# Performance work log

Measured on AMD Instinct MI355X. Metric: run time of the kernel, lower is better.

The kernel has to match this reference:

```python
import jax, jax.numpy as jnp
import numpy as np

N, D = 16384, 2048

def setup_inputs() -> dict:
    key = jax.random.key(0)
    k1, k2 = jax.random.split(key)
    F = jax.random.normal(k1, (N, D), dtype=jnp.float32)
    F_star = jax.random.normal(k2, (N, D), dtype=jnp.float32)
    lambda_r = jnp.float32(1.0)
    return {"F": F, "F_star": F_star, "lambda_r": lambda_r}

def reference(F, F_star, lambda_r):
    # trace(F F^T Fs Fs^T) == ||F^T Fs||_F^2 (cyclic trace property);
    # avoids materializing the n x n Gram matrices the torch code forms.
    G = jnp.einsum('nd,ne->de', F, F_star)  # [D, D]
    return lambda_r * jnp.sum(G * G)
```

## Files before the change

### kernel.cpp

```cpp
#include <hip/hip_runtime.h>
#include <hip/hip_bf16.h>

#define N_ROWS 16384
#define D_DIM  2048
#define SPLITK 4
#define NS     (N_ROWS / 32)
#define NP     (D_DIM / 128)
#define NSS    (NS / SPLITK)
#define NKT    (NSS / 2)


typedef __attribute__((ext_vector_type(8))) short short8;
typedef __attribute__((ext_vector_type(4))) float f32x4;
typedef __attribute__((ext_vector_type(8))) unsigned short ushort8;
typedef __attribute__((ext_vector_type(4))) unsigned short ushort4v;

#define GPTR(p) ((const __attribute__((address_space(1))) void*)(p))
#define LPTR(p) ((__attribute__((address_space(3))) void*)(p))

__device__ __forceinline__ unsigned short f2bf(float x) {
  __hip_bfloat16 b = __float2bfloat16(x);
  return *reinterpret_cast<unsigned short*>(&b);
}
__device__ __forceinline__ float bf2f(unsigned short u) {
  unsigned int v = ((unsigned int)u) << 16;
  return *reinterpret_cast<float*>(&v);
}

__global__ void __launch_bounds__(256) transpose_pack(
    const float* __restrict__ F, const float* __restrict__ Fs,
    unsigned short* __restrict__ Fb, unsigned short* __restrict__ Fsb) {
  const float* src = blockIdx.y ? Fs : F;
  unsigned short* dst = blockIdx.y ? Fsb : Fb;
  const int t = threadIdx.x;
  const int kb0 = blockIdx.x * 64;

  const int mg   = t & 31;
  const int koct = (t >> 5) & 3;
  const int c    = t >> 7;
  const int krow = kb0 + c * 32 + koct * 8;
  const int ks   = blockIdx.x * 2 + c;

  const float* srow = &src[(size_t)krow * D_DIM + mg * 4];
  unsigned short* obase = dst + (size_t)ks * 4096
                        + (size_t)(mg >> 2) * 512 + (size_t)koct * 128
                        + (size_t)(mg & 3) * 32;

#define LOADP(R, MT) do {                                                      \
    _Pragma("unroll") for (int j = 0; j < 8; ++j)                              \
      (R)[j] = *(const float4*)&srow[(size_t)j * D_DIM + (MT) * 128];          \
  } while (0)
#define STOREP(R, MT) do {                                                     \
    const float* _rp = (const float*)(R);                                      \
    unsigned short* _b = obase + (size_t)(MT) * (NS * 4096);                   \
    _Pragma("unroll") for (int i = 0; i < 4; ++i) {                            \
      ushort8 _o;                                                              \
      _Pragma("unroll") for (int j = 0; j < 8; ++j) _o[j] = f2bf(_rp[j*4+i]);  \
      *(ushort8*)&_b[i * 8] = _o;                                              \
    }                                                                          \
  } while (0)

  float4 rA[8], rB[8];
  LOADP(rA, 0);
#pragma unroll
  for (int mt = 0; mt < NP; mt += 2) {
    LOADP(rB, mt + 1);
    STOREP(rA, mt);
    if (mt + 2 < NP) LOADP(rA, mt + 2);
    STOREP(rB, mt + 1);
  }
#undef LOADP
#undef STOREP
}

__global__ void __launch_bounds__(512, 2) gemm_packed(
    const unsigned short* __restrict__ Fb, const unsigned short* __restrict__ Fsb,
    unsigned short* __restrict__ Cpart) {
  __shared__ unsigned short lds[65536];
  const int tid = threadIdx.x;
  const int w = tid >> 6, lane = tid & 63;
  const int wm = w >> 2, wn = w & 3;
  const int bx = blockIdx.x, by = blockIdx.y, z = blockIdx.z;

  const size_t kbase = (size_t)z * NSS * 4096;
  size_t aSrc0 = ((size_t)(by * 2 + 0) * NS) * 4096 + kbase + (size_t)w * 1024 + lane * 8;
  size_t aSrc1 = ((size_t)(by * 2 + 1) * NS) * 4096 + kbase + (size_t)w * 1024 + lane * 8;
  size_t bSrc0 = ((size_t)(bx * 2 + 0) * NS) * 4096 + kbase + (size_t)w * 1024 + lane * 8;
  size_t bSrc1 = ((size_t)(bx * 2 + 1) * NS) * 4096 + kbase + (size_t)w * 1024 + lane * 8;

  const int aRd = wm * 8192 + lane * 8;
  const int bRd = (wn >> 1) * 8192 + (wn & 1) * 2048 + lane * 8;

#define STAGE_A(KT, P, BUF) do {                                               \
    int _kt = (KT); if (_kt >= NKT) _kt -= NKT;                                \
    const unsigned short* _s = Fb + (P ? aSrc1 : aSrc0) + (size_t)_kt * 8192;  \
    unsigned short* _d = &lds[(BUF) * 16384 + (P) * 8192 + w * 1024];          \
    __builtin_amdgcn_global_load_lds(GPTR(_s),       LPTR(_d),       16, 0, 0);\
    __builtin_amdgcn_global_load_lds(GPTR(_s + 512), LPTR(_d + 512), 16, 0, 0);\
  } while (0)
#define STAGE_B(KT, Q, BUF) do {                                               \
    int _kt = (KT); if (_kt >= NKT) _kt -= NKT;                                \
    const unsigned short* _s = Fsb + (Q ? bSrc1 : bSrc0) + (size_t)_kt * 8192; \
    unsigned short* _d = &lds[32768 + (BUF) * 16384 + (Q) * 8192 + w * 1024];  \
    __builtin_amdgcn_global_load_lds(GPTR(_s),       LPTR(_d),       16, 0, 0);\
    __builtin_amdgcn_global_load_lds(GPTR(_s + 512), LPTR(_d + 512), 16, 0, 0);\
  } while (0)
#define LDA(DST, BUF, I, SL) (DST) = *(const short8*)&lds[(BUF) * 16384 + aRd + (SL) * 4096 + (I) * 512]
#define LDB(DST, BUF, J, SL) (DST) = *(const short8*)&lds[32768 + (BUF) * 16384 + bRd + (SL) * 4096 + (J) * 512]

  f32x4 acc[8][4];
#pragma unroll
  for (int i = 0; i < 8; ++i)
#pragma unroll
    for (int j = 0; j < 4; ++j) acc[i][j] = 0.f;

  short8 aR[4][2], bLo[2][2], bHi[2][2];

  STAGE_A(0, 0, 0); STAGE_A(0, 1, 0);
  STAGE_B(0, 0, 0); STAGE_B(0, 1, 0);
  STAGE_B(1, 0, 1); STAGE_B(1, 1, 1);
  asm volatile("s_waitcnt vmcnt(4)" ::: "memory");
  __builtin_amdgcn_s_barrier();

#define PHASE1(T, B) do {                                                      \
    _Pragma("unroll") for (int i = 0; i < 4; ++i) {                            \
      LDA(aR[i][0], B, i, 0); LDA(aR[i][1], B, i, 1); }                        \
    _Pragma("unroll") for (int j = 0; j < 2; ++j) {                            \
      LDB(bLo[j][0], B, j, 0); LDB(bLo[j][1], B, j, 1); }                      \
    STAGE_A((T) + 1, 0, (B) ^ 1);                                              \
    asm volatile("s_waitcnt lgkmcnt(8)" ::: "memory");                         \
    __builtin_amdgcn_s_barrier();                                              \
    asm volatile("s_waitcnt lgkmcnt(0)" ::: "memory");                         \
    __builtin_amdgcn_s_setprio(1);                                             \
    _Pragma("unroll") for (int sl = 0; sl < 2; ++sl)                           \
      _Pragma("unroll") for (int i = 0; i < 4; ++i)                            \
        _Pragma("unroll") for (int j = 0; j < 2; ++j)                          \
          acc[i][j] = __builtin_amdgcn_mfma_f32_16x16x32_bf16(aR[i][sl], bLo[j][sl], acc[i][j], 0, 0, 0); \
    __builtin_amdgcn_s_setprio(0);                                             \
    __builtin_amdgcn_s_barrier();                                              \
  } while (0)
#define PHASE2(T, B) do {                                                      \
    _Pragma("unroll") for (int j = 0; j < 2; ++j) {                            \
      LDB(bHi[j][0], B, 2 + j, 0); LDB(bHi[j][1], B, 2 + j, 1); }              \
    STAGE_A((T) + 1, 1, (B) ^ 1);                                              \
    __builtin_amdgcn_s_barrier();                                              \
    asm volatile("s_waitcnt lgkmcnt(0)" ::: "memory");                         \
    __builtin_amdgcn_s_setprio(1);                                             \
    _Pragma("unroll") for (int sl = 0; sl < 2; ++sl)                           \
      _Pragma("unroll") for (int i = 0; i < 4; ++i)                            \
        _Pragma("unroll") for (int j = 0; j < 2; ++j)                          \
          acc[i][2 + j] = __builtin_amdgcn_mfma_f32_16x16x32_bf16(aR[i][sl], bHi[j][sl], acc[i][2 + j], 0, 0, 0); \
    __builtin_amdgcn_s_setprio(0);                                             \
    __builtin_amdgcn_s_barrier();                                              \
  } while (0)
#define PHASE3(T, B) do {                                                      \
    _Pragma("unroll") for (int i = 0; i < 4; ++i) {                            \
      LDA(aR[i][0], B, 4 + i, 0); LDA(aR[i][1], B, 4 + i, 1); }                \
    STAGE_B((T) + 2, 0, B);                                                    \
    __builtin_amdgcn_s_barrier();                                              \
    asm volatile("s_waitcnt lgkmcnt(0)" ::: "memory");                         \
    __builtin_amdgcn_s_setprio(1);                                             \
    _Pragma("unroll") for (int sl = 0; sl < 2; ++sl)                           \
      _Pragma("unroll") for (int i = 0; i < 4; ++i)                            \
        _Pragma("unroll") for (int j = 0; j < 2; ++j)                          \
          acc[4 + i][2 + j] = __builtin_amdgcn_mfma_f32_16x16x32_bf16(aR[i][sl], bHi[j][sl], acc[4 + i][2 + j], 0, 0, 0); \
    __builtin_amdgcn_s_setprio(0);                                             \
    __builtin_amdgcn_s_barrier();                                              \
  } while (0)
#define PHASE4(T, B) do {                                                      \
    STAGE_B((T) + 2, 1, B);                                                    \
    __builtin_amdgcn_s_barrier();                                              \
    asm volatile("s_waitcnt lgkmcnt(0)" ::: "memory");                         \
    __builtin_amdgcn_s_setprio(1);                                             \
    _Pragma("unroll") for (int sl = 0; sl < 2; ++sl)                           \
      _Pragma("unroll") for (int i = 0; i < 4; ++i)                            \
        _Pragma("unroll") for (int j = 0; j < 2; ++j)                          \
          acc[4 + i][j] = __builtin_amdgcn_mfma_f32_16x16x32_bf16(aR[i][sl], bLo[j][sl], acc[4 + i][j], 0, 0, 0); \
    __builtin_amdgcn_s_setprio(0);                                             \
    asm volatile("s_waitcnt vmcnt(4)" ::: "memory");                           \
    __builtin_amdgcn_s_barrier();                                              \
  } while (0)

  for (int t = 0; t < NKT; t += 2) {
    PHASE1(t, 0); PHASE2(t, 0); PHASE3(t, 0); PHASE4(t, 0);
    PHASE1(t + 1, 1); PHASE2(t + 1, 1); PHASE3(t + 1, 1); PHASE4(t + 1, 1);
  }

  unsigned short* cp = Cpart + (size_t)z * (D_DIM * D_DIM)
                     + (size_t)(by * 8 + bx) * 65536 + w * 8192 + lane * 4;
#pragma unroll
  for (int i = 0; i < 8; ++i)
#pragma unroll
    for (int j = 0; j < 4; ++j) {
      ushort4v o;
#pragma unroll
      for (int r = 0; r < 4; ++r) o[r] = f2bf(acc[i][j][r]);
      *(ushort4v*)&cp[(i * 4 + j) * 256] = o;
    }
#undef STAGE_A
#undef STAGE_B
#undef LDA
#undef LDB
#undef PHASE1
#undef PHASE2
#undef PHASE3
#undef PHASE4
}

__global__ void __launch_bounds__(256) reduce_squares(
    const unsigned short* __restrict__ Cpart, const float* __restrict__ lam,
    float* __restrict__ out) {
  const int NQ = (D_DIM * D_DIM) / 8;
  const ushort8* c = (const ushort8*)Cpart;
  float s = 0.f;
  for (int idx = blockIdx.x * 256 + threadIdx.x; idx < NQ; idx += gridDim.x * 256) {
    float v[8];
#pragma unroll
    for (int j = 0; j < 8; ++j) v[j] = 0.f;
#pragma unroll
    for (int z = 0; z < SPLITK; ++z) {
      ushort8 u = c[(size_t)z * NQ + idx];
#pragma unroll
      for (int j = 0; j < 8; ++j) v[j] += bf2f(u[j]);
    }
#pragma unroll
    for (int j = 0; j < 8; ++j) s += v[j] * v[j];
  }
  for (int off = 32; off > 0; off >>= 1) s += __shfl_down(s, off, 64);
  __shared__ float red[4];
  const int wave = threadIdx.x >> 6, lane = threadIdx.x & 63;
  if (lane == 0) red[wave] = s;
  __syncthreads();
  if (threadIdx.x == 0) atomicAdd(out, (red[0] + red[1] + red[2] + red[3]) * lam[0]);
}

__global__ void __launch_bounds__(256) fallback_kernel(
    const float* __restrict__ F, const float* __restrict__ Fs,
    const float* __restrict__ lam, float* __restrict__ out) {
  __shared__ float sA[64][16], sB[64][16];
  const int d0 = blockIdx.y * 16, e0 = blockIdx.x * 16;
  const int t = threadIdx.x;
  const int td = t >> 4, te = t & 15;
  float s = 0.f;
  for (int k0 = 0; k0 < N_ROWS; k0 += 64) {
#pragma unroll
    for (int p = 0; p < 4; ++p) {
      const int k = (t >> 4) + p * 16;
      const int cc = t & 15;
      sA[k][cc] = F[(size_t)(k0 + k) * D_DIM + d0 + cc];
      sB[k][cc] = Fs[(size_t)(k0 + k) * D_DIM + e0 + cc];
    }
    __syncthreads();
#pragma unroll
    for (int kk = 0; kk < 64; ++kk) s += sA[kk][td] * sB[kk][te];
    __syncthreads();
  }
  float q = s * s;
  for (int off = 32; off > 0; off >>= 1) q += __shfl_down(q, off, 64);
  __shared__ float red[4];
  if ((t & 63) == 0) red[t >> 6] = q;
  __syncthreads();
  if (t == 0) atomicAdd(out, (red[0] + red[1] + red[2] + red[3]) * lam[0]);
}

extern "C" void kernel_launch(void* const* d_in, const int* in_sizes, int n_in,
                              void* d_out, int out_size, void* d_ws, size_t ws_size,
                              hipStream_t stream) {
  const float* F   = (const float*)d_in[0];
  const float* Fs  = (const float*)d_in[1];
  const float* lam = (const float*)d_in[2];
  float* out = (float*)d_out;
  hipMemsetAsync(d_out, 0, sizeof(float) * (size_t)out_size, stream);

  const size_t bf_bytes = (size_t)NP * NS * 8192;
  const size_t cpart_bytes = (size_t)SPLITK * D_DIM * D_DIM * 2;
  const size_t need = 2 * bf_bytes + cpart_bytes;

  if (ws_size >= need) {
    unsigned short* Fb  = (unsigned short*)d_ws;
    unsigned short* Fsb = Fb + bf_bytes / 2;
    unsigned short* Cpart = (unsigned short*)((char*)d_ws + 2 * bf_bytes);
    transpose_pack<<<dim3(N_ROWS / 64, 2), 256, 0, stream>>>(F, Fs, Fb, Fsb);
    gemm_packed<<<dim3(8, 8, SPLITK), 512, 0, stream>>>(Fb, Fsb, Cpart);
    reduce_squares<<<dim3(1024), 256, 0, stream>>>(Cpart, lam, out);
  } else {
    fallback_kernel<<<dim3(128, 128), 256, 0, stream>>>(F, Fs, lam, out);
  }
}
```

Before: 420.8 us.

## Restructure GEMM mainloop into two-phase tile schedule with block swizzle

```diff
diff --git a/kernel.cpp b/kernel.cpp
--- a/kernel.cpp
+++ b/kernel.cpp
@@ -46,10 +46,6 @@
                         + (size_t)(mg >> 2) * 512 + (size_t)koct * 128
                         + (size_t)(mg & 3) * 32;
 
-#define LOADP(R, MT) do {                                                      \
-    _Pragma("unroll") for (int j = 0; j < 8; ++j)                              \
-      (R)[j] = *(const float4*)&srow[(size_t)j * D_DIM + (MT) * 128];          \
-  } while (0)
 #define STOREP(R, MT) do {                                                     \
     const float* _rp = (const float*)(R);                                      \
     unsigned short* _b = obase + (size_t)(MT) * (NS * 4096);                   \
@@ -60,16 +56,16 @@
     }                                                                          \
   } while (0)
 
-  float4 rA[8], rB[8];
-  LOADP(rA, 0);
-#pragma unroll
   for (int mt = 0; mt < NP; mt += 2) {
-    LOADP(rB, mt + 1);
-    STOREP(rA, mt);
-    if (mt + 2 < NP) LOADP(rA, mt + 2);
-    STOREP(rB, mt + 1);
-  }
-#undef LOADP
+    float4 r0[8], r1[8];
+#pragma unroll
+    for (int j = 0; j < 8; ++j) {
+      r0[j] = *(const float4*)&srow[(size_t)j * D_DIM + mt * 128];
+      r1[j] = *(const float4*)&srow[(size_t)j * D_DIM + mt * 128 + 128];
+    }
+    STOREP(r0, mt);
+    STOREP(r1, mt + 1);
+  }
 #undef STOREP
 }
 
@@ -80,7 +76,10 @@
   const int tid = threadIdx.x;
   const int w = tid >> 6, lane = tid & 63;
   const int wm = w >> 2, wn = w & 3;
-  const int bx = blockIdx.x, by = blockIdx.y, z = blockIdx.z;
+
+  const int lin = blockIdx.x + (blockIdx.y << 3) + ((int)blockIdx.z << 6);
+  const int l   = (lin & 7) * 32 + (lin >> 3);
+  const int bx = l & 7, by = (l >> 3) & 7, z = l >> 6;
 
   const size_t kbase = (size_t)z * NSS * 4096;
   size_t aSrc0 = ((size_t)(by * 2 + 0) * NS) * 4096 + kbase + (size_t)w * 1024 + lane * 8;
@@ -114,76 +113,49 @@
 #pragma unroll
     for (int j = 0; j < 4; ++j) acc[i][j] = 0.f;
 
-  short8 aR[4][2], bLo[2][2], bHi[2][2];
+  short8 aR[8][2], bLo[2][2], bHi[2][2];
 
   STAGE_A(0, 0, 0); STAGE_A(0, 1, 0);
   STAGE_B(0, 0, 0); STAGE_B(0, 1, 0);
   STAGE_B(1, 0, 1); STAGE_B(1, 1, 1);
   asm volatile("s_waitcnt vmcnt(4)" ::: "memory");
   __builtin_amdgcn_s_barrier();
-
-#define PHASE1(T, B) do {                                                      \
-    _Pragma("unroll") for (int i = 0; i < 4; ++i) {                            \
+  __builtin_amdgcn_sched_barrier(0);
+
+#define TILE(T, B) do {                                                        \
+    STAGE_A((T) + 1, 0, (B) ^ 1);                                              \
+    STAGE_A((T) + 1, 1, (B) ^ 1);                                              \
+    _Pragma("unroll") for (int i = 0; i < 8; ++i) {                            \
       LDA(aR[i][0], B, i, 0); LDA(aR[i][1], B, i, 1); }                        \
     _Pragma("unroll") for (int j = 0; j < 2; ++j) {                            \
       LDB(bLo[j][0], B, j, 0); LDB(bLo[j][1], B, j, 1); }                      \
-    STAGE_A((T) + 1, 0, (B) ^ 1);                                              \
-    asm volatile("s_waitcnt lgkmcnt(8)" ::: "memory");                         \
-    __builtin_amdgcn_s_barrier();                                              \
-    asm volatile("s_waitcnt lgkmcnt(0)" ::: "memory");                         \
+    _Pragma("unroll") for (int j = 0; j < 2; ++j) {                            \
+      LDB(bHi[j][0], B, 2 + j, 0); LDB(bHi[j][1], B, 2 + j, 1); }              \
     __builtin_amdgcn_s_setprio(1);                                             \
     _Pragma("unroll") for (int sl = 0; sl < 2; ++sl)                           \
-      _Pragma("unroll") for (int i = 0; i < 4; ++i)                            \
+      _Pragma("unroll") for (int i = 0; i < 8; ++i)                            \
         _Pragma("unroll") for (int j = 0; j < 2; ++j)                          \
           acc[i][j] = __builtin_amdgcn_mfma_f32_16x16x32_bf16(aR[i][sl], bLo[j][sl], acc[i][j], 0, 0, 0); \
     __builtin_amdgcn_s_setprio(0);                                             \
+    asm volatile("s_waitcnt lgkmcnt(0)" ::: "memory");                         \
     __builtin_amdgcn_s_barrier();                                              \
-  } while (0)
-#define PHASE2(T, B) do {                                                      \
-    _Pragma("unroll") for (int j = 0; j < 2; ++j) {                            \
-      LDB(bHi[j][0], B, 2 + j, 0); LDB(bHi[j][1], B, 2 + j, 1); }              \
-    STAGE_A((T) + 1, 1, (B) ^ 1);                                              \
-    __builtin_amdgcn_s_barrier();                                              \
-    asm volatile("s_waitcnt lgkmcnt(0)" ::: "memory");                         \
+    __builtin_amdgcn_sched_barrier(0);                                         \
+    STAGE_B((T) + 2, 0, B);                                                    \
+    STAGE_B((T) + 2, 1, B);                                                    \
     __builtin_amdgcn_s_setprio(1);                                             \
     _Pragma("unroll") for (int sl = 0; sl < 2; ++sl)                           \
-      _Pragma("unroll") for (int i = 0; i < 4; ++i)                            \
+      _Pragma("unroll") for (int i = 0; i < 8; ++i)                            \
         _Pragma("unroll") for (int j = 0; j < 2; ++j)                          \
           acc[i][2 + j] = __builtin_amdgcn_mfma_f32_16x16x32_bf16(aR[i][sl], bHi[j][sl], acc[i][2 + j], 0, 0, 0); \
     __builtin_amdgcn_s_setprio(0);                                             \
-    __builtin_amdgcn_s_barrier();                                              \
-  } while (0)
-#define PHASE3(T, B) do {                                                      \
-    _Pragma("unroll") for (int i = 0; i < 4; ++i) {                            \
-      LDA(aR[i][0], B, 4 + i, 0); LDA(aR[i][1], B, 4 + i, 1); }                \
-    STAGE_B((T) + 2, 0, B);                                                    \
-    __builtin_amdgcn_s_barrier();                                              \
-    asm volatile("s_waitcnt lgkmcnt(0)" ::: "memory");                         \
-    __builtin_amdgcn_s_setprio(1);                                             \
-    _Pragma("unroll") for (int sl = 0; sl < 2; ++sl)                           \
-      _Pragma("unroll") for (int i = 0; i < 4; ++i)                            \
-        _Pragma("unroll") for (int j = 0; j < 2; ++j)                          \
-          acc[4 + i][2 + j] = __builtin_amdgcn_mfma_f32_16x16x32_bf16(aR[i][sl], bHi[j][sl], acc[4 + i][2 + j], 0, 0, 0); \
-    __builtin_amdgcn_s_setprio(0);                                             \
-    __builtin_amdgcn_s_barrier();                                              \
-  } while (0)
-#define PHASE4(T, B) do {                                                      \
-    STAGE_B((T) + 2, 1, B);                                                    \
-    __builtin_amdgcn_s_barrier();                                              \
-    asm volatile("s_waitcnt lgkmcnt(0)" ::: "memory");                         \
-    __builtin_amdgcn_s_setprio(1);                                             \
-    _Pragma("unroll") for (int sl = 0; sl < 2; ++sl)                           \
-      _Pragma("unroll") for (int i = 0; i < 4; ++i)                            \
-        _Pragma("unroll") for (int j = 0; j < 2; ++j)                          \
-          acc[4 + i][j] = __builtin_amdgcn_mfma_f32_16x16x32_bf16(aR[i][sl], bLo[j][sl], acc[4 + i][j], 0, 0, 0); \
-    __builtin_amdgcn_s_setprio(0);                                             \
     asm volatile("s_waitcnt vmcnt(4)" ::: "memory");                           \
     __builtin_amdgcn_s_barrier();                                              \
+    __builtin_amdgcn_sched_barrier(0);                                         \
   } while (0)
 
   for (int t = 0; t < NKT; t += 2) {
-    PHASE1(t, 0); PHASE2(t, 0); PHASE3(t, 0); PHASE4(t, 0);
-    PHASE1(t + 1, 1); PHASE2(t + 1, 1); PHASE3(t + 1, 1); PHASE4(t + 1, 1);
+    TILE(t, 0);
+    TILE(t + 1, 1);
   }
 
   unsigned short* cp = Cpart + (size_t)z * (D_DIM * D_DIM)
@@ -201,10 +173,7 @@
 #undef STAGE_B
 #undef LDA
 #undef LDB
-#undef PHASE1
-#undef PHASE2
-#undef PHASE3
-#undef PHASE4
+#undef TILE
 }
 
 __global__ void __launch_bounds__(256) reduce_squares(
```

Measured after the change: 544.6 us. +29.4%, slower.
